# Kernel optimization log

Hardware: AMD Instinct MI355X
Metric: run time of the kernel (lower is better)

The kernel has to match this reference:

```python
import jax, jax.numpy as jnp
import numpy as np
import math

T_SCALE = 99
FEAT_DIM = 400
BATCH = 2
C = 256
NH = 8
NS = 32
NSPB = 3
RATIO = 0.5
LOCAL_STEP = 33


def build_sample_mask(T=T_SCALE, ns=NS, nspb=NSPB, ratio=RATIO):
    # Vectorized port of _get_interp1d_mask. Flat layout: [time, (bin, start, end)].
    N = ns * nspb
    e_idx, s_idx = np.meshgrid(np.arange(T), np.arange(T), indexing='ij')
    valid = s_idx < e_idx
    starts_i = s_idx[valid].astype(np.int64)
    ends_i = e_idx[valid].astype(np.int64)
    starts = starts_i.astype(np.float64)
    ends = ends_i.astype(np.float64)
    center = ends - starts + 1.0
    xmin = starts - center * ratio
    plen = (ends + center * ratio) - xmin
    S = xmin[:, None] + (plen / (N - 1.0))[:, None] * np.arange(N)[None, :]  # [P, N]
    down = np.trunc(S).astype(np.int64)  # matches int(math.modf(s)[1]) (trunc toward 0)
    dec = S - down                       # can be negative when s < 0, as in the original
    up = np.ceil(S).astype(np.int64)
    bin_col = (np.arange(N) // nspb)[None, :] * (T * T) + (starts_i * T + ends_i)[:, None]
    M = np.zeros(T * ns * T * T, np.float64)
    vd = (down >= 0) & (down <= T - 1)
    np.add.at(M, (down * (ns * T * T) + bin_col)[vd], ((1.0 - dec) / nspb)[vd])
    vu = (up >= 0) & (up <= T - 1)
    np.add.at(M, (up * (ns * T * T) + bin_col)[vu], (dec / nspb)[vu])
    return M.reshape(T, ns * T * T).astype(np.float32)


def pos_ebb(scale, size):
    pos = jnp.arange(scale, dtype=jnp.float32)[:, None]
    div = jnp.exp(jnp.arange(0, size, 2, dtype=jnp.float32) * (-math.log(10000.0) / size))
    ang = pos * div
    # interleave sin (even) / cos (odd)
    return jnp.stack([jnp.sin(ang), jnp.cos(ang)], axis=-1).reshape(scale, size)


def layer_norm(x, g, b, eps=1e-5):
    mu = jnp.mean(x, -1, keepdims=True)
    var = jnp.mean((x - mu) ** 2, -1, keepdims=True)
    return (x - mu) * jax.lax.rsqrt(var + eps) * g + b


def mha(x, w_qkv, b_qkv, w_o, b_o, nh=NH):
    t, b, c = x.shape
    hd = c // nh
    q, k, v = jnp.split(x @ w_qkv.T + b_qkv, 3, axis=-1)
    q = q.reshape(t, b, nh, hd)
    k = k.reshape(t, b, nh, hd)
    v = v.reshape(t, b, nh, hd)
    att = jnp.einsum('qbhd,kbhd->bhqk', q, k) / math.sqrt(hd)
    att = jax.nn.softmax(att, axis=-1)
    o = jnp.einsum('bhqk,kbhd->qbhd', att, v).reshape(t, b, c)
    return o @ w_o.T + b_o


def encoder(x, p):
    # PyTorch post-norm TransformerEncoder (eval mode, dropout off) + final LayerNorm
    (qkv_w, qkv_b, o_w, o_b, l1_w, l1_b, l2_w, l2_b, n1_g, n1_b, n2_g, n2_b, nf_g, nf_b) = p
    for i in range(qkv_w.shape[0]):
        a = mha(x, qkv_w[i], qkv_b[i], o_w[i], o_b[i])
        x = layer_norm(x + a, n1_g[i], n1_b[i])
        f = jax.nn.relu(x @ l1_w[i].T + l1_b[i]) @ l2_w[i].T + l2_b[i]
        x = layer_norm(x + f, n2_g[i], n2_b[i])
    return layer_norm(x, nf_g, nf_b)


def conv1d(x, w, b, pad, groups=1):
    y = jax.lax.conv_general_dilated(x, w, (1,), [(pad, pad)],
                                     dimension_numbers=('NCH', 'OIH', 'NCH'),
                                     feature_group_count=groups)
    return y + b[None, :, None]


def conv2d(x, w, b, pad):
    y = jax.lax.conv_general_dilated(x, w, (1, 1), [(pad, pad), (pad, pad)],
                                     dimension_numbers=('NCHW', 'OIHW', 'NCHW'))
    return y + b[None, :, None, None]


def conv3d(x, w, b, stride):
    y = jax.lax.conv_general_dilated(x, w, stride, [(0, 0)] * 3,
                                     dimension_numbers=('NCDHW', 'OIDHW', 'NCDHW'))
    return y + b[None, :, None, None, None]


def _forward(x, cb_w, cb_b, tg_qkv_w, tg_qkv_b, tg_o_w, tg_o_b, tg_l1_w, tg_l1_b, tg_l2_w, tg_l2_b, tg_n1_g, tg_n1_b, tg_n2_g, tg_n2_b, tg_nf_g, tg_nf_b, tl_qkv_w, tl_qkv_b, tl_o_w, tl_o_b, tl_l1_w, tl_l1_b, tl_l2_w, tl_l2_b, tl_n1_g, tl_n1_b, tl_n2_g, tl_n2_b, tl_nf_g, tl_nf_b, s1_w, s1_b, s2_w, s2_b, c3_w, c3_b, p1_w, p1_b, p2_w, p2_b, p3_w, p3_b, sample_mask):
    B, _, T = x.shape
    base = jax.nn.relu(conv1d(x, cb_w, cb_b, pad=1, groups=4))  # [B,C,T]
    # local transformer on LOCAL_STEP-strided windows
    group = T // LOCAL_STEP
    tl_p = (tl_qkv_w, tl_qkv_b, tl_o_w, tl_o_b, tl_l1_w, tl_l1_b, tl_l2_w, tl_l2_b, tl_n1_g, tl_n1_b, tl_n2_g, tl_n2_b, tl_nf_g, tl_nf_b)
    feat = base.reshape(B, C, LOCAL_STEP, group).transpose(2, 3, 0, 1).reshape(LOCAL_STEP, B * group, C)
    feat = encoder(feat + pos_ebb(LOCAL_STEP, C)[:, None, :], tl_p)
    local = feat.reshape(LOCAL_STEP * group, B, C).transpose(1, 2, 0)  # [B,C,T]
    # global bidirectional transformer (shared weights, flipped second pass)
    tg_p = (tg_qkv_w, tg_qkv_b, tg_o_w, tg_o_b, tg_l1_w, tg_l1_b, tg_l2_w, tg_l2_b, tg_n1_g, tg_n1_b, tg_n2_g, tg_n2_b, tg_nf_g, tg_nf_b)
    g = base.transpose(2, 0, 1)  # [T,B,C]
    pe = pos_ebb(T, C)[:, None, :]
    f1 = encoder(g + pe, tg_p)
    f2 = encoder(g[::-1] + pe, tg_p)
    base2 = local + (f1 + f2[::-1]).transpose(1, 2, 0)  # [B,C,T]
    s = jax.nn.relu(conv1d(base2, s1_w, s1_b, pad=1, groups=4))
    start1 = jax.nn.sigmoid(conv1d(s, s2_w, s2_b, pad=0))[:, 0, :]  # [B,T]
    # boundary-matching layer: dense matmul against precomputed interp mask
    bm = jnp.matmul(base2, sample_mask).reshape(B, C, NS, T, T)
    p = jax.nn.relu(conv3d(bm, c3_w, c3_b, (NS, 1, 1)))[:, :, 0]  # [B,C,T,T]
    p = jax.nn.relu(conv2d(p, p1_w, p1_b, pad=1))
    p = jax.nn.relu(conv2d(p, p2_w, p2_b, pad=1))
    cm = jax.nn.sigmoid(conv2d(p, p3_w, p3_b, pad=0))  # [B,2,T,T]
    return cm, start1


def setup_inputs() -> dict:
    key = jax.random.key(0)
    ks = iter(jax.random.split(key, 80))
    def rnd(shape):
        return 0.02 * jax.random.normal(next(ks), shape, dtype=jnp.float32)
    inp = {'x': jax.random.normal(next(ks), (BATCH, FEAT_DIM, T_SCALE), dtype=jnp.float32)}
    inp['cb_w'] = rnd((C, FEAT_DIM // 4, 3)); inp['cb_b'] = jnp.zeros((C,), jnp.float32)
    for pre, n in (('tg', 6), ('tl', 3)):
        inp[pre + '_qkv_w'] = rnd((n, 3 * C, C)); inp[pre + '_qkv_b'] = jnp.zeros((n, 3 * C), jnp.float32)
        inp[pre + '_o_w'] = rnd((n, C, C)); inp[pre + '_o_b'] = jnp.zeros((n, C), jnp.float32)
        inp[pre + '_l1_w'] = rnd((n, 1024, C)); inp[pre + '_l1_b'] = jnp.zeros((n, 1024), jnp.float32)
        inp[pre + '_l2_w'] = rnd((n, C, 1024)); inp[pre + '_l2_b'] = jnp.zeros((n, C), jnp.float32)
        inp[pre + '_n1_g'] = jnp.ones((n, C), jnp.float32); inp[pre + '_n1_b'] = jnp.zeros((n, C), jnp.float32)
        inp[pre + '_n2_g'] = jnp.ones((n, C), jnp.float32); inp[pre + '_n2_b'] = jnp.zeros((n, C), jnp.float32)
        inp[pre + '_nf_g'] = jnp.ones((C,), jnp.float32); inp[pre + '_nf_b'] = jnp.zeros((C,), jnp.float32)
    inp['s1_w'] = rnd((C, C // 4, 3)); inp['s1_b'] = jnp.zeros((C,), jnp.float32)
    inp['s2_w'] = rnd((1, C, 1)); inp['s2_b'] = jnp.zeros((1,), jnp.float32)
    inp['c3_w'] = rnd((C, C, NS, 1, 1)); inp['c3_b'] = jnp.zeros((C,), jnp.float32)
    inp['p1_w'] = rnd((C, C, 3, 3)); inp['p1_b'] = jnp.zeros((C,), jnp.float32)
    inp['p2_w'] = rnd((C, C, 3, 3)); inp['p2_b'] = jnp.zeros((C,), jnp.float32)
    inp['p3_w'] = rnd((2, C, 1, 1)); inp['p3_b'] = jnp.zeros((2,), jnp.float32)
    inp['sample_mask'] = jnp.asarray(build_sample_mask())  # [T, NS*T*T], exact BMN interp mask
    return inp


def reference(x, cb_w, cb_b, tg_qkv_w, tg_qkv_b, tg_o_w, tg_o_b, tg_l1_w, tg_l1_b, tg_l2_w, tg_l2_b, tg_n1_g, tg_n1_b, tg_n2_g, tg_n2_b, tg_nf_g, tg_nf_b, tl_qkv_w, tl_qkv_b, tl_o_w, tl_o_b, tl_l1_w, tl_l1_b, tl_l2_w, tl_l2_b, tl_n1_g, tl_n1_b, tl_n2_g, tl_n2_b, tl_nf_g, tl_nf_b, s1_w, s1_b, s2_w, s2_b, c3_w, c3_b, p1_w, p1_b, p2_w, p2_b, p3_w, p3_b, sample_mask):
    return _forward(x, cb_w, cb_b, tg_qkv_w, tg_qkv_b, tg_o_w, tg_o_b, tg_l1_w, tg_l1_b, tg_l2_w, tg_l2_b, tg_n1_g, tg_n1_b, tg_n2_g, tg_n2_b, tg_nf_g, tg_nf_b, tl_qkv_w, tl_qkv_b, tl_o_w, tl_o_b, tl_l1_w, tl_l1_b, tl_l2_w, tl_l2_b, tl_n1_g, tl_n1_b, tl_n2_g, tl_n2_b, tl_nf_g, tl_nf_b, s1_w, s1_b, s2_w, s2_b, c3_w, c3_b, p1_w, p1_b, p2_w, p2_b, p3_w, p3_b, sample_mask)
```

## Files before the change

### kernel.cpp

```cpp
#include <hip/hip_runtime.h>
#include <math.h>

#define T99   99
#define CC    256
#define NHH   8
#define FEAT  400
#define NS_   32
#define LSTEP 33

typedef __attribute__((ext_vector_type(8))) short s8v;
typedef __attribute__((ext_vector_type(4))) float f4v;

__device__ __forceinline__ void mfma_bf16(f4v& d, s8v a, s8v b) {
  asm("v_mfma_f32_16x16x32_bf16 %0, %1, %2, %0" : "+v"(d) : "v"(a), "v"(b));
}

__device__ __forceinline__ unsigned short f2bf(float f) {
  union { float f; unsigned u; } x; x.f = f;
  unsigned r = x.u + 0x7FFFu + ((x.u >> 16) & 1u);
  return (unsigned short)(r >> 16);
}
__device__ __forceinline__ float bf2f(unsigned short h) {
  union { unsigned u; float f; } x; x.u = ((unsigned)h) << 16;
  return x.f;
}
__device__ __forceinline__ float blo(unsigned u) { union { unsigned x; float f; } c; c.x = u << 16; return c.f; }
__device__ __forceinline__ float bhi(unsigned u) { union { unsigned x; float f; } c; c.x = u & 0xffff0000u; return c.f; }

__device__ __forceinline__ float pe_val(int pos, int c) {
  int i = c >> 1;
  float freq = expf((float)(2 * i) * (-0.03597789207803197f));
  float ang = (float)pos * freq;
  return (c & 1) ? cosf(ang) : sinf(ang);
}

__global__ __launch_bounds__(128) void k_convbase(const float* __restrict__ x,
                                                  const float* __restrict__ w,
                                                  const float* __restrict__ bias,
                                                  float* __restrict__ base) {
  int b = blockIdx.x >> 8, co = blockIdx.x & 255, t = threadIdx.x;
  if (t >= T99) return;
  int g = co >> 6;
  float acc = bias[co];
  const float* xp = x + (size_t)(b * FEAT + g * 100) * T99;
  const float* wp = w + (size_t)co * 300;
  for (int ic = 0; ic < 100; ++ic) {
    float x0 = (t > 0)  ? xp[ic * T99 + t - 1] : 0.f;
    float x1 = xp[ic * T99 + t];
    float x2 = (t < 98) ? xp[ic * T99 + t + 1] : 0.f;
    acc += wp[ic * 3] * x0 + wp[ic * 3 + 1] * x1 + wp[ic * 3 + 2] * x2;
  }
  base[(size_t)(b * CC + co) * T99 + t] = fmaxf(acc, 0.f);
}

__global__ __launch_bounds__(256) void k_wpackF(const float* __restrict__ qkv, const float* __restrict__ o,
                                                const float* __restrict__ l1, const float* __restrict__ l2,
                                                int L, unsigned short* __restrict__ dst) {
  int idx = blockIdx.x * 256 + threadIdx.x;
  if (idx >= L * 98304) return;
  int l = idx / 98304, v = idx % 98304;
  const float* src;
  int N, K, lv;
  if (v < 24576)      { src = qkv + (size_t)l * 196608; N = 768;  K = 256;  lv = v; }
  else if (v < 32768) { src = o   + (size_t)l * 65536;  N = 256;  K = 256;  lv = v - 24576; }
  else if (v < 65536) { src = l1  + (size_t)l * 262144; N = 1024; K = 256;  lv = v - 32768; }
  else                { src = l2  + (size_t)l * 262144; N = 256;  K = 1024; lv = v - 65536; }
  int lane = lv & 63, r = lv >> 6;
  int nkst = K >> 5;
  int kst = r % nkst, cg = r / nkst;
  int co = cg * 16 + (lane & 15);
  int k  = kst * 32 + (lane >> 4) * 8;
  const float* sp = src + (size_t)co * K + k;
  s8v out;
#pragma unroll
  for (int q = 0; q < 8; ++q) out[q] = (short)f2bf(sp[q]);
  *(s8v*)&dst[(size_t)idx * 8] = out;
}

__global__ __launch_bounds__(256) void k_build_xg(const float* __restrict__ base, float* __restrict__ xg,
                                                  unsigned short* __restrict__ xgb) {
  int idx = blockIdx.x * 256 + threadIdx.x;
  int t = idx >> 10, r = idx & 1023, b4 = r >> 8, c = r & 255;
  float v = (b4 < 2) ? base[(size_t)(b4 * CC + c) * T99 + t]
                     : base[(size_t)((b4 - 2) * CC + c) * T99 + (98 - t)];
  v += pe_val(t, c);
  xg[idx] = v; xgb[idx] = f2bf(v);
}

__global__ __launch_bounds__(256) void k_build_xl(const float* __restrict__ base, float* __restrict__ xl,
                                                  unsigned short* __restrict__ xlb) {
  int idx = blockIdx.x * 256 + threadIdx.x;
  int ls = idx / 1536, r = idx % 1536, j = r >> 8, c = r & 255;
  int g = j >> 1, b = j & 1, t = ls * 3 + g;
  float v = base[(size_t)(b * CC + c) * T99 + t] + pe_val(ls, c);
  xl[idx] = v; xlb[idx] = f2bf(v);
}

struct GJ {
  const unsigned short* Ab;
  const unsigned short* Wf;
  const float* bias;
  const float* R;
  float* Yf;
  unsigned short* Yb;
  int M, N, K, flags;
};

__device__ __forceinline__ void g_body(const GJ& j, int m0, int n0) {
  __shared__ __align__(16) unsigned short Al[64][264];
  int tid = threadIdx.x, lane = tid & 63, w = tid >> 6, wm = w >> 1, wn = w & 1;
  f4v acc[2][2];
#pragma unroll
  for (int mt = 0; mt < 2; ++mt)
#pragma unroll
    for (int nt = 0; nt < 2; ++nt) acc[mt][nt] = (f4v){0.f, 0.f, 0.f, 0.f};
  int nkst = j.K >> 5;
  for (int kc0 = 0; kc0 < j.K; kc0 += 256) {
#pragma unroll
    for (int it = 0; it < 8; ++it) {
      int idx = it * 256 + tid, row = idx >> 5, seg = idx & 31;
      s8v av = {0, 0, 0, 0, 0, 0, 0, 0};
      if (m0 + row < j.M) av = *(const s8v*)&j.Ab[(size_t)(m0 + row) * j.K + kc0 + seg * 8];
      *(s8v*)&Al[row][seg * 8] = av;
    }
    __syncthreads();
    int kb = kc0 >> 5;
#pragma unroll
    for (int kst = 0; kst < 8; ++kst) {
      s8v af[2], bf[2];
#pragma unroll
      for (int mt = 0; mt < 2; ++mt)
        af[mt] = *(const s8v*)&Al[wm * 32 + mt * 16 + (lane & 15)][kst * 32 + (lane >> 4) * 8];
#pragma unroll
      for (int nt = 0; nt < 2; ++nt) {
        int cg = (n0 >> 4) + wn * 2 + nt;
        bf[nt] = *(const s8v*)&j.Wf[((size_t)(cg * nkst + kb + kst) * 64 + lane) * 8];
      }
#pragma unroll
      for (int mt = 0; mt < 2; ++mt)
#pragma unroll
        for (int nt = 0; nt < 2; ++nt) mfma_bf16(acc[mt][nt], af[mt], bf[nt]);
    }
    __syncthreads();
  }
  asm volatile("s_nop 7\n\ts_nop 7\n\ts_nop 4");
#pragma unroll
  for (int mt = 0; mt < 2; ++mt) {
#pragma unroll
    for (int nt = 0; nt < 2; ++nt) {
      int col = n0 + wn * 32 + nt * 16 + (lane & 15);
      float bv = j.bias[col];
#pragma unroll
      for (int r = 0; r < 4; ++r) {
        int row = m0 + wm * 32 + mt * 16 + (lane >> 4) * 4 + r;
        if (row < j.M) {
          float v = acc[mt][nt][r] + bv;
          if (j.flags & 2) v += j.R[(size_t)row * j.N + col];
          if (j.flags & 1) v = fmaxf(v, 0.f);
          if (!(j.flags & 8)) j.Yf[(size_t)row * j.N + col] = v;
          if (j.flags & 4) j.Yb[(size_t)row * j.N + col] = f2bf(v);
        }
      }
    }
  }
}

__global__ __launch_bounds__(256) void k_g(GJ j) {
  if ((int)blockIdx.x * 64 >= j.M) return;
  g_body(j, blockIdx.x * 64, blockIdx.y * 64);
}

__global__ __launch_bounds__(256) void k_g2(GJ j0, GJ j1) {
  if (blockIdx.z == 0) {
    if ((int)blockIdx.x * 64 >= j0.M) return;
    g_body(j0, blockIdx.x * 64, blockIdx.y * 64);
  } else {
    if ((int)blockIdx.x * 64 >= j1.M) return;
    g_body(j1, blockIdx.x * 64, blockIdx.y * 64);
  }
}

__device__ __forceinline__ void attn_body(const unsigned short* __restrict__ qkv,
                                          unsigned short* __restrict__ attb,
                                          int T_, int B_, int bid) {
  __shared__ float qv[32];
  __shared__ float red[128];
  __shared__ float pv[128];
  int tid = threadIdx.x;
  int q = bid % T_;
  int h = (bid / T_) % NHH;
  int b = bid / (T_ * NHH);
  if (tid < 32) qv[tid] = bf2f(qkv[(size_t)(q * B_ + b) * 768 + h * 32 + tid]);
  __syncthreads();
  float s = -1e30f;
  if (tid < T_) {
    const unsigned short* kp = qkv + (size_t)(tid * B_ + b) * 768 + 256 + h * 32;
    float d = 0;
#pragma unroll
    for (int i = 0; i < 32; ++i) d += qv[i] * bf2f(kp[i]);
    s = d * 0.176776695296636881f;
  }
  red[tid] = s; __syncthreads();
  for (int o = 64; o > 0; o >>= 1) { if (tid < o) red[tid] = fmaxf(red[tid], red[tid + o]); __syncthreads(); }
  float mx = red[0]; __syncthreads();
  float p = (tid < T_) ? expf(s - mx) : 0.f;
  pv[tid] = p; red[tid] = p; __syncthreads();
  for (int o = 64; o > 0; o >>= 1) { if (tid < o) red[tid] += red[tid + o]; __syncthreads(); }
  float denom = red[0];
  __syncthreads();
  int d = tid & 31, part = tid >> 5;
  float o = 0.f;
  for (int k = part; k < T_; k += 4)
    o += pv[k] * bf2f(qkv[(size_t)(k * B_ + b) * 768 + 512 + h * 32 + d]);
  red[tid] = o; __syncthreads();
  if (tid < 32) {
    float t = red[tid] + red[tid + 32] + red[tid + 64] + red[tid + 96];
    attb[(size_t)(q * B_ + b) * 256 + h * 32 + tid] = f2bf(t / denom);
  }
}

__global__ __launch_bounds__(128) void k_attn(const unsigned short* __restrict__ qkv,
                                              unsigned short* __restrict__ attb, int T_, int B_) {
  attn_body(qkv, attb, T_, B_, blockIdx.x);
}

__global__ __launch_bounds__(128) void k_attn2(const unsigned short* __restrict__ qkv0,
                                               unsigned short* __restrict__ attb0, int T0, int B0,
                                               const unsigned short* __restrict__ qkv1,
                                               unsigned short* __restrict__ attb1, int T1, int B1) {
  int bid = blockIdx.x;
  if (blockIdx.z == 0) {
    if (bid >= B0 * NHH * T0) return;
    attn_body(qkv0, attb0, T0, B0, bid);
  } else {
    if (bid >= B1 * NHH * T1) return;
    attn_body(qkv1, attb1, T1, B1, bid);
  }
}

__device__ __forceinline__ void ln_body(const float* __restrict__ X, const float* __restrict__ g,
                                        const float* __restrict__ bb, float* __restrict__ Y,
                                        unsigned short* __restrict__ Yb, int tok) {
  __shared__ float rs[256], rq[256];
  int c = threadIdx.x;
  float v = X[(size_t)tok * 256 + c];
  rs[c] = v; rq[c] = v * v; __syncthreads();
  for (int o = 128; o > 0; o >>= 1) { if (c < o) { rs[c] += rs[c + o]; rq[c] += rq[c + o]; } __syncthreads(); }
  float mu = rs[0] * (1.f / 256.f);
  float var = rq[0] * (1.f / 256.f) - mu * mu;
  float r = (v - mu) * rsqrtf(var + 1e-5f) * g[c] + bb[c];
  Y[(size_t)tok * 256 + c] = r;
  if (Yb) Yb[(size_t)tok * 256 + c] = f2bf(r);
}

__global__ __launch_bounds__(256) void k_ln(const float* __restrict__ X, const float* __restrict__ g,
                                            const float* __restrict__ bb, float* __restrict__ Y,
                                            unsigned short* __restrict__ Yb) {
  ln_body(X, g, bb, Y, Yb, blockIdx.x);
}

__global__ __launch_bounds__(256) void k_ln2(const float* __restrict__ X0, const float* __restrict__ g0,
                                             const float* __restrict__ bb0, float* __restrict__ Y0,
                                             unsigned short* __restrict__ Yb0, int n0,
                                             const float* __restrict__ X1, const float* __restrict__ g1,
                                             const float* __restrict__ bb1, float* __restrict__ Y1,
                                             unsigned short* __restrict__ Yb1, int n1) {
  int tok = blockIdx.x;
  if (blockIdx.z == 0) { if (tok < n0) ln_body(X0, g0, bb0, Y0, Yb0, tok); }
  else                 { if (tok < n1) ln_body(X1, g1, bb1, Y1, Yb1, tok); }
}

__global__ __launch_bounds__(256) void k_combine(const float* __restrict__ encl, const float* __restrict__ encg,
                                                 float* __restrict__ base2) {
  int idx = blockIdx.x * 256 + threadIdx.x;
  int t = idx % T99, c = (idx / T99) & 255, b = idx / (CC * T99);
  int ls = t / 3, g = t % 3;
  float v = encl[(size_t)(ls * 6 + g * 2 + b) * 256 + c]
          + encg[(size_t)(t * 4 + b) * 256 + c]
          + encg[(size_t)((98 - t) * 4 + 2 + b) * 256 + c];
  base2[idx] = v;
}

__global__ __launch_bounds__(256) void k_sfuse(const float* __restrict__ base2, const float* __restrict__ s1w,
                                               const float* __restrict__ s1b, const float* __restrict__ s2w,
                                               const float* __restrict__ s2b, float* __restrict__ out) {
  __shared__ float rs[256];
  int b = blockIdx.x / T99, t = blockIdx.x % T99, co = threadIdx.x;
  int g = co >> 6;
  float acc = s1b[co];
  const float* xp = base2 + (size_t)(b * CC + g * 64) * T99;
  const float* wp = s1w + (size_t)co * 192;
  for (int ic = 0; ic < 64; ++ic) {
    float x0 = (t > 0)  ? xp[ic * T99 + t - 1] : 0.f;
    float x1 = xp[ic * T99 + t];
    float x2 = (t < 98) ? xp[ic * T99 + t + 1] : 0.f;
    acc += wp[ic * 3] * x0 + wp[ic * 3 + 1] * x1 + wp[ic * 3 + 2] * x2;
  }
  rs[co] = fmaxf(acc, 0.f) * s2w[co];
  __syncthreads();
  for (int o = 128; o > 0; o >>= 1) { if (co < o) rs[co] += rs[co + o]; __syncthreads(); }
  if (co == 0) out[blockIdx.x] = 1.f / (1.f + expf(-(rs[0] + s2b[0])));
}

__global__ __launch_bounds__(256) void k_w3t(const float* __restrict__ c3w, float* __restrict__ w3t) {
  int idx = blockIdx.x * 256 + threadIdx.x;
  int co = idx & 255, ci = (idx >> 8) & 255, n = idx >> 16;
  w3t[idx] = c3w[((size_t)(co << 8) + ci) * 32 + n];
}

__global__ __launch_bounds__(256) void k_G(const float* __restrict__ w3t, const float* __restrict__ base2,
                                           unsigned short* __restrict__ Gb) {
  int tc = blockIdx.x, n = blockIdx.y, b = blockIdx.z;
  int co = threadIdx.x;
  int t0 = tc * 25;
  float acc[25];
#pragma unroll
  for (int q = 0; q < 25; ++q) acc[q] = 0.f;
  const float* w = w3t + (size_t)n * 65536 + co;
  const float* bs = base2 + (size_t)b * CC * T99 + t0;
  for (int ci = 0; ci < 256; ++ci) {
    float wv = w[(size_t)ci * 256];
#pragma unroll
    for (int q = 0; q < 25; ++q) acc[q] += wv * bs[ci * T99 + q];
  }
#pragma unroll
  for (int q = 0; q < 25; ++q) {
    int t = t0 + q;
    if (t < T99) Gb[((size_t)(n * T99 + t) * 256 + co) * 2 + b] = f2bf(acc[q]);
  }
  if (tc == 0 && n == 0 && b == 0)
    ((unsigned int*)(Gb + (size_t)NS_ * T99 * 512))[co] = 0u;
}

__global__ __launch_bounds__(256) void k_ppre(const unsigned short* __restrict__ Gb,
                                              const float* __restrict__ c3b,
                                              unsigned int* __restrict__ pinb32) {
  __shared__ float w0s[96], w1s[96];
  __shared__ int   ofs[96];
  __shared__ float part[128][4];
  int e = blockIdx.x % T99, s = blockIdx.x / T99;
  int tid = threadIdx.x;
  if (s >= e) {
    if (tid < 128) {
      float z0 = fmaxf(c3b[2 * tid], 0.f), z1 = fmaxf(c3b[2 * tid + 1], 0.f);
      unsigned int zz = ((unsigned)f2bf(z1) << 16) | (unsigned)f2bf(z0);
      pinb32[((size_t)s * T99 + e) * 128 + tid] = zz;
      pinb32[((size_t)(T99 + s) * T99 + e) * 128 + tid] = zz;
    }
    return;
  }
  if (tid < 96) {
    double center = (double)(e - s + 1);
    double S = ((double)s - 0.5 * center) + ((2.0 * center - 1.0) / 95.0) * (double)tid;
    double dn = trunc(S);
    double dec = S - dn;
    int di = (int)dn;
    double uc = ceil(S);
    int ui = (int)uc;
    int n = tid / 3;
    float w0 = 0.f, w1 = 0.f;
    int r0 = 0;
    if (dn >= 0.0 && dn <= 98.0) {
      r0 = di;
      w0 = (float)((1.0 - dec) / 3.0);
      if (uc >= 0.0 && uc <= 98.0) {
        if (ui == di) w0 += (float)(dec / 3.0);
        else          w1  = (float)(dec / 3.0);
      }
    }
    w0s[tid] = w0; w1s[tid] = w1;
    ofs[tid] = (n * T99 + r0) * 1024;
  }
  __syncthreads();
  int ch = tid & 127, half = tid >> 7;
  float a00 = 0.f, a01 = 0.f, a10 = 0.f, a11 = 0.f;
  const char* basep = (const char*)Gb + ch * 8;
  int k0 = half * 48;
#pragma unroll 8
  for (int k = k0; k < k0 + 48; ++k) {
    float w0 = w0s[k], w1 = w1s[k];
    const uint2* p = (const uint2*)(basep + ofs[k]);
    uint2 u0 = p[0];
    uint2 u1 = p[128];
    a00 += w0 * blo(u0.x) + w1 * blo(u1.x);
    a01 += w0 * bhi(u0.x) + w1 * bhi(u1.x);
    a10 += w0 * blo(u0.y) + w1 * blo(u1.y);
    a11 += w0 * bhi(u0.y) + w1 * bhi(u1.y);
  }
  if (half) { part[ch][0] = a00; part[ch][1] = a01; part[ch][2] = a10; part[ch][3] = a11; }
  __syncthreads();
  if (tid < 128) {
    a00 += part[ch][0]; a01 += part[ch][1]; a10 += part[ch][2]; a11 += part[ch][3];
    float b0 = c3b[2 * tid], b1 = c3b[2 * tid + 1];
    unsigned int zb0 = ((unsigned)f2bf(fmaxf(a10 + b1, 0.f)) << 16) | (unsigned)f2bf(fmaxf(a00 + b0, 0.f));
    unsigned int zb1 = ((unsigned)f2bf(fmaxf(a11 + b1, 0.f)) << 16) | (unsigned)f2bf(fmaxf(a01 + b0, 0.f));
    pinb32[((size_t)s * T99 + e) * 128 + tid] = zb0;
    pinb32[((size_t)(T99 + s) * T99 + e) * 128 + tid] = zb1;
  }
}

__global__ __launch_bounds__(256) void k_wb2(const float* __restrict__ pw, unsigned short* __restrict__ wbf) {
  int idx = blockIdx.x * 256 + threadIdx.x;
  if (idx >= 73728) return;
  int lane = idx & 63;
  int cog  = (idx >> 6) & 15;
  int kst  = (idx >> 10) & 7;
  int tap  = idx >> 13;
  int co = cog * 16 + (lane & 15);
  int k  = kst * 32 + (lane >> 4) * 8;
  s8v v;
#pragma unroll
  for (int j = 0; j < 8; ++j)
    v[j] = (short)f2bf(pw[((size_t)co * 256 + k + j) * 9 + tap]);
  *(s8v*)&wbf[(size_t)idx * 8] = v;
}

__global__ __launch_bounds__(256) void k_cvec(const float* __restrict__ pw, const float* __restrict__ cin,
                                              const float* __restrict__ bias, int reluCin,
                                              float* __restrict__ coutF, unsigned short* __restrict__ coutB) {
  __shared__ float rs[256];
  int co = blockIdx.x, ci = threadIdx.x;
  float c = cin[ci];
  if (reluCin) c = fmaxf(c, 0.f);
  const float* wp = pw + ((size_t)co * 256 + ci) * 9;
  float wsum = 0.f;
#pragma unroll
  for (int t = 0; t < 9; ++t) wsum += wp[t];
  rs[ci] = wsum * c;
  __syncthreads();
  for (int o = 128; o > 0; o >>= 1) { if (ci < o) rs[ci] += rs[ci + o]; __syncthreads(); }
  if (ci == 0) {
    float r = fmaxf(bias[co] + rs[0], 0.f);
    coutF[co] = r;
    coutB[co] = f2bf(r);
  }
}

__device__ __forceinline__ int aoff(int s) {
  int tap = s >> 3, kst = s & 7;
  return ((tap / 3) * 10 + (tap % 3)) * 264 + kst * 32;
}
__device__ __forceinline__ void ldb4(const unsigned short* __restrict__ B0, int s, s8v* dst) {
#pragma unroll
  for (int nt = 0; nt < 4; ++nt) dst[nt] = *(const s8v*)(B0 + (size_t)s * 8192 + nt * 512);
}

__global__ __launch_bounds__(256) void k_conv3x3(const unsigned short* __restrict__ in,
                                                 const unsigned short* __restrict__ wbf,
                                                 const float* __restrict__ bias,
                                                 const unsigned short* __restrict__ cvecB,
                                                 int D, int lo, int hi,
                                                 unsigned short* __restrict__ out) {
  __shared__ __align__(16) unsigned short Ah[100 * 264];
  int b = blockIdx.z;
  int co0 = blockIdx.y * 128;
  int ti = blockIdx.x / 13, tj = blockIdx.x % 13;
  int i0 = ti * 8, j0 = tj * 8;
  int tid = threadIdx.x;

  if (i0 - 1 >= lo && i0 + 8 <= hi && j0 - 1 >= lo && j0 + 8 <= hi && i0 - 1 >= j0 + 8 + D) {
    const unsigned int* cv = (const unsigned int*)(cvecB + co0);
    unsigned int* ob = (unsigned int*)out;
#pragma unroll
    for (int r = 0; r < 16; ++r) {
      int idx = r * 256 + tid;
      int sp = idx >> 6, cp = idx & 63;
      int gi = i0 + (sp >> 3), gj = j0 + (sp & 7);
      ob[((size_t)(b * T99 + gi) * T99 + gj) * 128 + (co0 >> 1) + cp] = cv[cp];
    }
    return;
  }

#pragma unroll
  for (int it = 0; it < 13; ++it) {
    int chunk = it * 256 + tid;
    if (chunk < 3200) {
      int row = chunk >> 5;
      int cc = (chunk & 31) * 8;
      int gi = i0 + row / 10 - 1, gj = j0 + row % 10 - 1;
      s8v val = {0, 0, 0, 0, 0, 0, 0, 0};
      if (gi >= 0 && gi < T99 && gj >= 0 && gj < T99)
        val = *(const s8v*)&in[((size_t)(b * T99 + gi) * T99 + gj) * 256 + cc];
      *(s8v*)&Ah[row * 264 + cc] = val;
    }
  }
  __syncthreads();

  int lane = tid & 63, w = tid >> 6, wm = w >> 1, wn = w & 1;
  int l15 = lane & 15, lk = lane >> 4;
  int spL0 = wm * 32 + l15, spL1 = spL0 + 16;
  int hr0 = (spL0 >> 3) * 10 + (spL0 & 7);
  int hr1 = (spL1 >> 3) * 10 + (spL1 & 7);
  const unsigned short* A0 = &Ah[hr0 * 264 + lk * 8];
  const unsigned short* A1 = &Ah[hr1 * 264 + lk * 8];
  int cogbase = blockIdx.y * 8 + wn * 4;
  const unsigned short* B0 = wbf + (size_t)cogbase * 512 + (size_t)lane * 8;

  f4v acc[2][4];
#pragma unroll
  for (int mt = 0; mt < 2; ++mt)
#pragma unroll
    for (int nt = 0; nt < 4; ++nt) acc[mt][nt] = (f4v){0.f, 0.f, 0.f, 0.f};

  s8v a0c, a1c, a0n, a1n;
  s8v bq[3][4];
  a0c = *(const s8v*)(A0 + aoff(0));
  a1c = *(const s8v*)(A1 + aoff(0));
  a0n = a0c; a1n = a1c;
  ldb4(B0, 0, bq[0]);
  ldb4(B0, 1, bq[1]);
#pragma unroll
  for (int s = 0; s < 72; ++s) {
    if (s + 2 < 72) ldb4(B0, s + 2, bq[(s + 2) % 3]);
    if (s + 1 < 72) {
      a0n = *(const s8v*)(A0 + aoff(s + 1));
      a1n = *(const s8v*)(A1 + aoff(s + 1));
    }
#pragma unroll
    for (int nt = 0; nt < 4; ++nt) {
      mfma_bf16(acc[0][nt], a0c, bq[s % 3][nt]);
      mfma_bf16(acc[1][nt], a1c, bq[s % 3][nt]);
    }
    a0c = a0n; a1c = a1n;
  }

  asm volatile("s_nop 7\n\ts_nop 7\n\ts_nop 4");
#pragma unroll
  for (int mt = 0; mt < 2; ++mt) {
#pragma unroll
    for (int nt = 0; nt < 4; ++nt) {
      int co = co0 + wn * 64 + nt * 16 + l15;
      float bv = bias[co];
#pragma unroll
      for (int r = 0; r < 4; ++r) {
        int sp = wm * 32 + mt * 16 + lk * 4 + r;
        int gi = i0 + (sp >> 3), gj = j0 + (sp & 7);
        if (gi < T99 && gj < T99) {
          float v = fmaxf(acc[mt][nt][r] + bv, 0.f);
          out[((size_t)(b * T99 + gi) * T99 + gj) * 256 + co] = f2bf(v);
        }
      }
    }
  }
}

__global__ __launch_bounds__(256) void k_p3(const unsigned short* __restrict__ p2o,
                                            const float* __restrict__ w, const float* __restrict__ bias,
                                            float* __restrict__ cm) {
  int idx = blockIdx.x * 256 + threadIdx.x;
  if (idx >= 2 * T99 * T99) return;
  int j = idx % T99, i = (idx / T99) % T99, b = idx / (T99 * T99);
  float a0 = bias[0], a1 = bias[1];
  const unsigned short* row = p2o + ((size_t)(b * T99 + i) * T99 + j) * 256;
  for (int c8 = 0; c8 < 256; c8 += 8) {
    s8v v = *(const s8v*)&row[c8];
#pragma unroll
    for (int q = 0; q < 8; ++q) {
      float x = bf2f((unsigned short)v[q]);
      a0 += w[c8 + q] * x;
      a1 += w[256 + c8 + q] * x;
    }
  }
  size_t base = (size_t)b * 2 * T99 * T99 + (size_t)i * T99 + j;
  cm[base] = 1.f / (1.f + expf(-a0));
  cm[base + T99 * T99] = 1.f / (1.f + expf(-a1));
}

struct EncW {
  const float *qkvw, *qkvb, *ow, *ob, *l1w, *l1b, *l2w, *l2b, *n1g, *n1b, *n2g, *n2b, *nfg, *nfb;
};
struct EncBufs {
  float* x; unsigned short* xb;
  float* yb;
  unsigned short *qkvb, *attb, *hb;
  int M;
};

static GJ jqkv(const EncW& W, const unsigned short* Wp, int l, const EncBufs& B) {
  GJ j = {}; j.Ab = B.xb; j.Wf = Wp + (size_t)l * 786432;
  j.bias = W.qkvb + (size_t)l * 768; j.Yb = B.qkvb; j.flags = 4 | 8;
  j.M = B.M; j.N = 768; j.K = 256; return j;
}
static GJ jproj(const EncW& W, const unsigned short* Wp, int l, const EncBufs& B) {
  GJ j = {}; j.Ab = B.attb; j.Wf = Wp + (size_t)l * 786432 + 196608;
  j.bias = W.ob + (size_t)l * 256; j.R = B.x; j.Yf = B.yb; j.flags = 2;
  j.M = B.M; j.N = 256; j.K = 256; return j;
}
static GJ jffn1(const EncW& W, const unsigned short* Wp, int l, const EncBufs& B) {
  GJ j = {}; j.Ab = B.xb; j.Wf = Wp + (size_t)l * 786432 + 262144;
  j.bias = W.l1b + (size_t)l * 1024; j.Yb = B.hb; j.flags = 1 | 4 | 8;
  j.M = B.M; j.N = 1024; j.K = 256; return j;
}
static GJ jffn2(const EncW& W, const unsigned short* Wp, int l, const EncBufs& B) {
  GJ j = {}; j.Ab = B.hb; j.Wf = Wp + (size_t)l * 786432 + 524288;
  j.bias = W.l2b + (size_t)l * 256; j.R = B.x; j.Yf = B.yb; j.flags = 2;
  j.M = B.M; j.N = 256; j.K = 1024; return j;
}

extern "C" void kernel_launch(void* const* d_in, const int* in_sizes, int n_in,
                              void* d_out, int out_size, void* d_ws, size_t ws_size,
                              hipStream_t stream) {
  (void)in_sizes; (void)n_in; (void)out_size; (void)ws_size;
  const float* x    = (const float*)d_in[0];
  const float* cbw  = (const float*)d_in[1];
  const float* cbb  = (const float*)d_in[2];
  EncW tg = {(const float*)d_in[3],  (const float*)d_in[4],  (const float*)d_in[5],  (const float*)d_in[6],
             (const float*)d_in[7],  (const float*)d_in[8],  (const float*)d_in[9],  (const float*)d_in[10],
             (const float*)d_in[11], (const float*)d_in[12], (const float*)d_in[13], (const float*)d_in[14],
             (const float*)d_in[15], (const float*)d_in[16]};
  EncW tl = {(const float*)d_in[17], (const float*)d_in[18], (const float*)d_in[19], (const float*)d_in[20],
             (const float*)d_in[21], (const float*)d_in[22], (const float*)d_in[23], (const float*)d_in[24],
             (const float*)d_in[25], (const float*)d_in[26], (const float*)d_in[27], (const float*)d_in[28],
             (const float*)d_in[29], (const float*)d_in[30]};
  const float* s1w = (const float*)d_in[31];
  const float* s1b = (const float*)d_in[32];
  const float* s2w = (const float*)d_in[33];
  const float* s2b = (const float*)d_in[34];
  const float* c3w = (const float*)d_in[35];
  const float* c3b = (const float*)d_in[36];
  const float* p1w = (const float*)d_in[37];
  const float* p1b = (const float*)d_in[38];
  const float* p2w = (const float*)d_in[39];
  const float* p2b = (const float*)d_in[40];
  const float* p3w = (const float*)d_in[41];
  const float* p3b = (const float*)d_in[42];

  float* outp = (float*)d_out;

  char* wp = (char*)d_ws;
  auto alloc = [&](size_t bytes) -> void* {
    void* p = (void*)wp;
    wp += (bytes + 255) & ~(size_t)255;
    return p;
  };
  float* base  = (float*)alloc(sizeof(float) * 2 * CC * T99);
  const int ML = 198, MG = 396;
  EncBufs BG, BL;
  BG.M = MG; BL.M = ML;
  BG.x  = (float*)alloc(sizeof(float) * MG * 256);
  BL.x  = (float*)alloc(sizeof(float) * ML * 256);
  BG.xb = (unsigned short*)alloc(sizeof(short) * MG * 256);
  BL.xb = (unsigned short*)alloc(sizeof(short) * ML * 256);
  BG.yb = (float*)alloc(sizeof(float) * MG * 256);
  BL.yb = (float*)alloc(sizeof(float) * ML * 256);
  BG.qkvb = (unsigned short*)alloc(sizeof(short) * MG * 768);
  BL.qkvb = (unsigned short*)alloc(sizeof(short) * ML * 768);
  BG.attb = (unsigned short*)alloc(sizeof(short) * MG * 256);
  BL.attb = (unsigned short*)alloc(sizeof(short) * ML * 256);
  BG.hb = (unsigned short*)alloc(sizeof(short) * MG * 1024);
  BL.hb = (unsigned short*)alloc(sizeof(short) * ML * 1024);
  float* encg  = (float*)alloc(sizeof(float) * MG * 256);
  float* encl  = (float*)alloc(sizeof(float) * ML * 256);
  float* base2 = (float*)alloc(sizeof(float) * 2 * CC * T99);
  float* w3t   = (float*)alloc(sizeof(float) * 32 * 256 * 256);
  unsigned short* Gb = (unsigned short*)alloc(sizeof(short) * (2 * NS_ * T99 * 256 + 512));
  unsigned short* pinb = (unsigned short*)alloc(sizeof(short) * 2 * T99 * T99 * 256);
  unsigned short* p1o  = (unsigned short*)alloc(sizeof(short) * 2 * T99 * T99 * 256);
  unsigned short* p2o  = (unsigned short*)alloc(sizeof(short) * 2 * T99 * T99 * 256);
  unsigned short* wb2a = (unsigned short*)alloc(sizeof(short) * 9 * 256 * 256);
  unsigned short* wb2b = (unsigned short*)alloc(sizeof(short) * 9 * 256 * 256);
  unsigned short* wpg  = (unsigned short*)alloc(sizeof(short) * 6 * 786432);
  unsigned short* wpl  = (unsigned short*)alloc(sizeof(short) * 3 * 786432);
  float* c1F = (float*)alloc(sizeof(float) * 256);
  unsigned short* c1B = (unsigned short*)alloc(sizeof(short) * 256);
  float* c2F = (float*)alloc(sizeof(float) * 256);
  unsigned short* c2B = (unsigned short*)alloc(sizeof(short) * 256);

  k_wpackF<<<dim3(2304), dim3(256), 0, stream>>>(tg.qkvw, tg.ow, tg.l1w, tg.l2w, 6, wpg);
  k_wpackF<<<dim3(1152), dim3(256), 0, stream>>>(tl.qkvw, tl.ow, tl.l1w, tl.l2w, 3, wpl);
  k_w3t<<<dim3(8192), dim3(256), 0, stream>>>(c3w, w3t);
  k_wb2<<<dim3(288), dim3(256), 0, stream>>>(p1w, wb2a);
  k_wb2<<<dim3(288), dim3(256), 0, stream>>>(p2w, wb2b);
  k_cvec<<<dim3(256), dim3(256), 0, stream>>>(p1w, c3b, p1b, 1, c1F, c1B);
  k_cvec<<<dim3(256), dim3(256), 0, stream>>>(p2w, c1F, p2b, 0, c2F, c2B);
  k_convbase<<<dim3(512), dim3(128), 0, stream>>>(x, cbw, cbb, base);
  k_build_xl<<<dim3(198), dim3(256), 0, stream>>>(base, BL.x, BL.xb);
  k_build_xg<<<dim3(396), dim3(256), 0, stream>>>(base, BG.x, BG.xb);

  const int mgG = 7;
  for (int l = 0; l < 3; ++l) {
    k_g2<<<dim3(mgG, 12, 2), dim3(256), 0, stream>>>(jqkv(tl, wpl, l, BL), jqkv(tg, wpg, l, BG));
    k_attn2<<<dim3(4 * NHH * T99, 1, 2), dim3(128), 0, stream>>>(BL.qkvb, BL.attb, LSTEP, 6,
                                                                 BG.qkvb, BG.attb, T99, 4);
    k_g2<<<dim3(mgG, 4, 2), dim3(256), 0, stream>>>(jproj(tl, wpl, l, BL), jproj(tg, wpg, l, BG));
    k_ln2<<<dim3(MG, 1, 2), dim3(256), 0, stream>>>(BL.yb, tl.n1g + l * 256, tl.n1b + l * 256, BL.x, BL.xb, ML,
                                                    BG.yb, tg.n1g + l * 256, tg.n1b + l * 256, BG.x, BG.xb, MG);
    k_g2<<<dim3(mgG, 16, 2), dim3(256), 0, stream>>>(jffn1(tl, wpl, l, BL), jffn1(tg, wpg, l, BG));
    k_g2<<<dim3(mgG, 4, 2), dim3(256), 0, stream>>>(jffn2(tl, wpl, l, BL), jffn2(tg, wpg, l, BG));
    k_ln2<<<dim3(MG, 1, 2), dim3(256), 0, stream>>>(BL.yb, tl.n2g + l * 256, tl.n2b + l * 256, BL.x, BL.xb, ML,
                                                    BG.yb, tg.n2g + l * 256, tg.n2b + l * 256, BG.x, BG.xb, MG);
  }
  for (int l = 3; l < 6; ++l) {
    k_g<<<dim3(mgG, 12), dim3(256), 0, stream>>>(jqkv(tg, wpg, l, BG));
    k_attn<<<dim3(4 * NHH * T99), dim3(128), 0, stream>>>(BG.qkvb, BG.attb, T99, 4);
    k_g<<<dim3(mgG, 4), dim3(256), 0, stream>>>(jproj(tg, wpg, l, BG));
    k_ln<<<dim3(MG), dim3(256), 0, stream>>>(BG.yb, tg.n1g + l * 256, tg.n1b + l * 256, BG.x, BG.xb);
    k_g<<<dim3(mgG, 16), dim3(256), 0, stream>>>(jffn1(tg, wpg, l, BG));
    k_g<<<dim3(mgG, 4), dim3(256), 0, stream>>>(jffn2(tg, wpg, l, BG));
    k_ln<<<dim3(MG), dim3(256), 0, stream>>>(BG.yb, tg.n2g + l * 256, tg.n2b + l * 256, BG.x, BG.xb);
  }
  k_ln2<<<dim3(MG, 1, 2), dim3(256), 0, stream>>>(BL.x, tl.nfg, tl.nfb, encl, nullptr, ML,
                                                  BG.x, tg.nfg, tg.nfb, encg, nullptr, MG);
  k_combine<<<dim3(198), dim3(256), 0, stream>>>(encl, encg, base2);
  k_sfuse<<<dim3(198), dim3(256), 0, stream>>>(base2, s1w, s1b, s2w, s2b, outp + 2 * 2 * T99 * T99);
  k_G<<<dim3(4, 32, 2), dim3(256), 0, stream>>>(w3t, base2, Gb);
  k_ppre<<<dim3(T99 * T99), dim3(256), 0, stream>>>(Gb, c3b, (unsigned int*)pinb);
  k_conv3x3<<<dim3(169, 2, 2), dim3(256), 0, stream>>>(pinb, wb2a, p1b, c1B, 0, 0, 98, p1o);
  k_conv3x3<<<dim3(169, 2, 2), dim3(256), 0, stream>>>(p1o, wb2b, p2b, c2B, 2, 1, 97, p2o);
  k_p3<<<dim3(77), dim3(256), 0, stream>>>(p2o, p3w, p3b, outp);
}
```

Measured before the change: 756.6 us.

## Stage row-major bf16 weights through shared memory instead of MFMA-prepacked layout

Replaces the MFMA fragment-prepacked weight conversion with a plain row-major fp32-to-bf16 conversion in a grid-stride kernel. The GEMM body now stages a 64x256 weight tile in a second shared-memory buffer and reads B fragments from LDS, rather than loading prepacked fragments straight from global memory. g_body also loses forceinline. The simpler packing kernel may be cheaper, but each GEMM block now uses twice the shared memory and does an extra LDS round trip, which can lower occupancy.

```diff
diff --git a/kernel.cpp b/kernel.cpp
--- a/kernel.cpp
+++ b/kernel.cpp
@@ -53,28 +53,19 @@
   base[(size_t)(b * CC + co) * T99 + t] = fmaxf(acc, 0.f);
 }
 
-__global__ __launch_bounds__(256) void k_wpackF(const float* __restrict__ qkv, const float* __restrict__ o,
-                                                const float* __restrict__ l1, const float* __restrict__ l2,
-                                                int L, unsigned short* __restrict__ dst) {
-  int idx = blockIdx.x * 256 + threadIdx.x;
-  if (idx >= L * 98304) return;
-  int l = idx / 98304, v = idx % 98304;
-  const float* src;
-  int N, K, lv;
-  if (v < 24576)      { src = qkv + (size_t)l * 196608; N = 768;  K = 256;  lv = v; }
-  else if (v < 32768) { src = o   + (size_t)l * 65536;  N = 256;  K = 256;  lv = v - 24576; }
-  else if (v < 65536) { src = l1  + (size_t)l * 262144; N = 1024; K = 256;  lv = v - 32768; }
-  else                { src = l2  + (size_t)l * 262144; N = 256;  K = 1024; lv = v - 65536; }
-  int lane = lv & 63, r = lv >> 6;
-  int nkst = K >> 5;
-  int kst = r % nkst, cg = r / nkst;
-  int co = cg * 16 + (lane & 15);
-  int k  = kst * 32 + (lane >> 4) * 8;
-  const float* sp = src + (size_t)co * K + k;
-  s8v out;
-#pragma unroll
-  for (int q = 0; q < 8; ++q) out[q] = (short)f2bf(sp[q]);
-  *(s8v*)&dst[(size_t)idx * 8] = out;
+__global__ __launch_bounds__(256) void k_convW(const float* __restrict__ qkv, const float* __restrict__ o,
+                                               const float* __restrict__ l1, const float* __restrict__ l2,
+                                               int L, unsigned short* __restrict__ dst) {
+  int total = L * 786432;
+  for (int idx = blockIdx.x * 256 + threadIdx.x; idx < total; idx += gridDim.x * 256) {
+    int l = idx / 786432, r = idx % 786432;
+    float v;
+    if (r < 196608)      v = qkv[(size_t)l * 196608 + r];
+    else if (r < 262144) v = o[(size_t)l * 65536 + (r - 196608)];
+    else if (r < 524288) v = l1[(size_t)l * 262144 + (r - 262144)];
+    else                 v = l2[(size_t)l * 262144 + (r - 524288)];
+    dst[idx] = f2bf(v);
+  }
 }
 
 __global__ __launch_bounds__(256) void k_build_xg(const float* __restrict__ base, float* __restrict__ xg,
@@ -98,7 +89,7 @@
 
 struct GJ {
   const unsigned short* Ab;
-  const unsigned short* Wf;
+  const unsigned short* W;
   const float* bias;
   const float* R;
   float* Yf;
@@ -106,36 +97,36 @@
   int M, N, K, flags;
 };
 
-__device__ __forceinline__ void g_body(const GJ& j, int m0, int n0) {
+__device__ void g_body(const GJ& j, int m0, int n0) {
   __shared__ __align__(16) unsigned short Al[64][264];
+  __shared__ __align__(16) unsigned short Bl[64][264];
   int tid = threadIdx.x, lane = tid & 63, w = tid >> 6, wm = w >> 1, wn = w & 1;
   f4v acc[2][2];
 #pragma unroll
   for (int mt = 0; mt < 2; ++mt)
 #pragma unroll
     for (int nt = 0; nt < 2; ++nt) acc[mt][nt] = (f4v){0.f, 0.f, 0.f, 0.f};
-  int nkst = j.K >> 5;
+
   for (int kc0 = 0; kc0 < j.K; kc0 += 256) {
 #pragma unroll
     for (int it = 0; it < 8; ++it) {
-      int idx = it * 256 + tid, row = idx >> 5, seg = idx & 31;
+      int idx = it * 256 + tid, row = idx >> 5, seg = (idx & 31) << 3;
       s8v av = {0, 0, 0, 0, 0, 0, 0, 0};
-      if (m0 + row < j.M) av = *(const s8v*)&j.Ab[(size_t)(m0 + row) * j.K + kc0 + seg * 8];
-      *(s8v*)&Al[row][seg * 8] = av;
+      if (m0 + row < j.M) av = *(const s8v*)&j.Ab[(size_t)(m0 + row) * j.K + kc0 + seg];
+      *(s8v*)&Al[row][seg] = av;
+      *(s8v*)&Bl[row][seg] = *(const s8v*)&j.W[(size_t)(n0 + row) * j.K + kc0 + seg];
     }
     __syncthreads();
-    int kb = kc0 >> 5;
 #pragma unroll
     for (int kst = 0; kst < 8; ++kst) {
+      int kcol = kst * 32 + (lane >> 4) * 8;
       s8v af[2], bf[2];
 #pragma unroll
       for (int mt = 0; mt < 2; ++mt)
-        af[mt] = *(const s8v*)&Al[wm * 32 + mt * 16 + (lane & 15)][kst * 32 + (lane >> 4) * 8];
-#pragma unroll
-      for (int nt = 0; nt < 2; ++nt) {
-        int cg = (n0 >> 4) + wn * 2 + nt;
-        bf[nt] = *(const s8v*)&j.Wf[((size_t)(cg * nkst + kb + kst) * 64 + lane) * 8];
-      }
+        af[mt] = *(const s8v*)&Al[wm * 32 + mt * 16 + (lane & 15)][kcol];
+#pragma unroll
+      for (int nt = 0; nt < 2; ++nt)
+        bf[nt] = *(const s8v*)&Bl[wn * 32 + nt * 16 + (lane & 15)][kcol];
 #pragma unroll
       for (int mt = 0; mt < 2; ++mt)
 #pragma unroll
@@ -576,23 +567,23 @@
   int M;
 };
 
-static GJ jqkv(const EncW& W, const unsigned short* Wp, int l, const EncBufs& B) {
-  GJ j = {}; j.Ab = B.xb; j.Wf = Wp + (size_t)l * 786432;
+static GJ jqkv(const EncW& W, const unsigned short* Wb, int l, const EncBufs& B) {
+  GJ j = {}; j.Ab = B.xb; j.W = Wb + (size_t)l * 786432;
   j.bias = W.qkvb + (size_t)l * 768; j.Yb = B.qkvb; j.flags = 4 | 8;
   j.M = B.M; j.N = 768; j.K = 256; return j;
 }
-static GJ jproj(const EncW& W, const unsigned short* Wp, int l, const EncBufs& B) {
-  GJ j = {}; j.Ab = B.attb; j.Wf = Wp + (size_t)l * 786432 + 196608;
+static GJ jproj(const EncW& W, const unsigned short* Wb, int l, const EncBufs& B) {
+  GJ j = {}; j.Ab = B.attb; j.W = Wb + (size_t)l * 786432 + 196608;
   j.bias = W.ob + (size_t)l * 256; j.R = B.x; j.Yf = B.yb; j.flags = 2;
   j.M = B.M; j.N = 256; j.K = 256; return j;
 }
-static GJ jffn1(const EncW& W, const unsigned short* Wp, int l, const EncBufs& B) {
-  GJ j = {}; j.Ab = B.xb; j.Wf = Wp + (size_t)l * 786432 + 262144;
+static GJ jffn1(const EncW& W, const unsigned short* Wb, int l, const EncBufs& B) {
+  GJ j = {}; j.Ab = B.xb; j.W = Wb + (size_t)l * 786432 + 262144;
   j.bias = W.l1b + (size_t)l * 1024; j.Yb = B.hb; j.flags = 1 | 4 | 8;
   j.M = B.M; j.N = 1024; j.K = 256; return j;
 }
-static GJ jffn2(const EncW& W, const unsigned short* Wp, int l, const EncBufs& B) {
-  GJ j = {}; j.Ab = B.hb; j.Wf = Wp + (size_t)l * 786432 + 524288;
+static GJ jffn2(const EncW& W, const unsigned short* Wb, int l, const EncBufs& B) {
+  GJ j = {}; j.Ab = B.hb; j.W = Wb + (size_t)l * 786432 + 524288;
   j.bias = W.l2b + (size_t)l * 256; j.R = B.x; j.Yf = B.yb; j.flags = 2;
   j.M = B.M; j.N = 256; j.K = 1024; return j;
 }
@@ -659,15 +650,15 @@
   unsigned short* p2o  = (unsigned short*)alloc(sizeof(short) * 2 * T99 * T99 * 256);
   unsigned short* wb2a = (unsigned short*)alloc(sizeof(short) * 9 * 256 * 256);
   unsigned short* wb2b = (unsigned short*)alloc(sizeof(short) * 9 * 256 * 256);
-  unsigned short* wpg  = (unsigned short*)alloc(sizeof(short) * 6 * 786432);
-  unsigned short* wpl  = (unsigned short*)alloc(sizeof(short) * 3 * 786432);
+  unsigned short* wtgb = (unsigned short*)alloc(sizeof(short) * 6 * 786432);
+  unsigned short* wtlb = (unsigned short*)alloc(sizeof(short) * 3 * 786432);
   float* c1F = (float*)alloc(sizeof(float) * 256);
   unsigned short* c1B = (unsigned short*)alloc(sizeof(short) * 256);
   float* c2F = (float*)alloc(sizeof(float) * 256);
   unsigned short* c2B = (unsigned short*)alloc(sizeof(short) * 256);
 
-  k_wpackF<<<dim3(2304), dim3(256), 0, stream>>>(tg.qkvw, tg.ow, tg.l1w, tg.l2w, 6, wpg);
-  k_wpackF<<<dim3(1152), dim3(256), 0, stream>>>(tl.qkvw, tl.ow, tl.l1w, tl.l2w, 3, wpl);
+  k_convW<<<dim3(4096), dim3(256), 0, stream>>>(tg.qkvw, tg.ow, tg.l1w, tg.l2w, 6, wtgb);
+  k_convW<<<dim3(2048), dim3(256), 0, stream>>>(tl.qkvw, tl.ow, tl.l1w, tl.l2w, 3, wtlb);
   k_w3t<<<dim3(8192), dim3(256), 0, stream>>>(c3w, w3t);
   k_wb2<<<dim3(288), dim3(256), 0, stream>>>(p1w, wb2a);
   k_wb2<<<dim3(288), dim3(256), 0, stream>>>(p2w, wb2b);
@@ -679,24 +670,24 @@
 
   const int mgG = 7;
   for (int l = 0; l < 3; ++l) {
-    k_g2<<<dim3(mgG, 12, 2), dim3(256), 0, stream>>>(jqkv(tl, wpl, l, BL), jqkv(tg, wpg, l, BG));
+    k_g2<<<dim3(mgG, 12, 2), dim3(256), 0, stream>>>(jqkv(tl, wtlb, l, BL), jqkv(tg, wtgb, l, BG));
     k_attn2<<<dim3(4 * NHH * T99, 1, 2), dim3(128), 0, stream>>>(BL.qkvb, BL.attb, LSTEP, 6,
                                                                  BG.qkvb, BG.attb, T99, 4);
-    k_g2<<<dim3(mgG, 4, 2), dim3(256), 0, stream>>>(jproj(tl, wpl, l, BL), jproj(tg, wpg, l, BG));
+    k_g2<<<dim3(mgG, 4, 2), dim3(256), 0, stream>>>(jproj(tl, wtlb, l, BL), jproj(tg, wtgb, l, BG));
     k_ln2<<<dim3(MG, 1, 2), dim3(256), 0, stream>>>(BL.yb, tl.n1g + l * 256, tl.n1b + l * 256, BL.x, BL.xb, ML,
                                                     BG.yb, tg.n1g + l * 256, tg.n1b + l * 256, BG.x, BG.xb, MG);
-    k_g2<<<dim3(mgG, 16, 2), dim3(256), 0, stream>>>(jffn1(tl, wpl, l, BL), jffn1(tg, wpg, l, BG));
-    k_g2<<<dim3(mgG, 4, 2), dim3(256), 0, stream>>>(jffn2(tl, wpl, l, BL), jffn2(tg, wpg, l, BG));
+    k_g2<<<dim3(mgG, 16, 2), dim3(256), 0, stream>>>(jffn1(tl, wtlb, l, BL), jffn1(tg, wtgb, l, BG));
+    k_g2<<<dim3(mgG, 4, 2), dim3(256), 0, stream>>>(jffn2(tl, wtlb, l, BL), jffn2(tg, wtgb, l, BG));
     k_ln2<<<dim3(MG, 1, 2), dim3(256), 0, stream>>>(BL.yb, tl.n2g + l * 256, tl.n2b + l * 256, BL.x, BL.xb, ML,
                                                     BG.yb, tg.n2g + l * 256, tg.n2b + l * 256, BG.x, BG.xb, MG);
   }
   for (int l = 3; l < 6; ++l) {
-    k_g<<<dim3(mgG, 12), dim3(256), 0, stream>>>(jqkv(tg, wpg, l, BG));
+    k_g<<<dim3(mgG, 12), dim3(256), 0, stream>>>(jqkv(tg, wtgb, l, BG));
     k_attn<<<dim3(4 * NHH * T99), dim3(128), 0, stream>>>(BG.qkvb, BG.attb, T99, 4);
-    k_g<<<dim3(mgG, 4), dim3(256), 0, stream>>>(jproj(tg, wpg, l, BG));
+    k_g<<<dim3(mgG, 4), dim3(256), 0, stream>>>(jproj(tg, wtgb, l, BG));
     k_ln<<<dim3(MG), dim3(256), 0, stream>>>(BG.yb, tg.n1g + l * 256, tg.n1b + l * 256, BG.x, BG.xb);
-    k_g<<<dim3(mgG, 16), dim3(256), 0, stream>>>(jffn1(tg, wpg, l, BG));
-    k_g<<<dim3(mgG, 4), dim3(256), 0, stream>>>(jffn2(tg, wpg, l, BG));
+    k_g<<<dim3(mgG, 16), dim3(256), 0, stream>>>(jffn1(tg, wtgb, l, BG));
+    k_g<<<dim3(mgG, 4), dim3(256), 0, stream>>>(jffn2(tg, wtgb, l, BG));
     k_ln<<<dim3(MG), dim3(256), 0, stream>>>(BG.yb, tg.n2g + l * 256, tg.n2b + l * 256, BG.x, BG.xb);
   }
   k_ln2<<<dim3(MG, 1, 2), dim3(256), 0, stream>>>(BL.x, tl.nfg, tl.nfb, encl, nullptr, ML,
```

Result: faster. 688.1 us (-9.0%).
